# Optimization experiments

Measured on AMD Instinct MI355X. Metric: run time of the kernel, lower is better.

## Reference

```python
import jax, jax.numpy as jnp
import numpy as np

N_NODES = 50000
N_EDGES = 800000
DIM = 64
BN_EPS = 1e-5


def setup_inputs() -> dict:
    key = jax.random.key(0)
    ks = jax.random.split(key, 9)
    s = 1.0 / np.sqrt(DIM)
    feature = jax.random.normal(ks[0], (N_NODES, DIM), jnp.float32)
    edge_index = jax.random.randint(ks[1], (2, N_EDGES), 0, N_NODES)
    Wk = jax.random.normal(ks[2], (DIM, DIM), jnp.float32) * s
    Wq = jax.random.normal(ks[3], (DIM, DIM), jnp.float32) * s
    Wv = jax.random.normal(ks[4], (DIM, DIM), jnp.float32) * s
    bk = jax.random.normal(ks[5], (DIM,), jnp.float32) * 0.01
    bq = jax.random.normal(ks[6], (DIM,), jnp.float32) * 0.01
    bv = jax.random.normal(ks[7], (DIM,), jnp.float32) * 0.01
    bias = jax.random.normal(ks[8], (DIM,), jnp.float32) * 0.01
    gamma = jnp.ones((DIM,), jnp.float32)
    beta = jnp.zeros((DIM,), jnp.float32)
    return dict(feature=feature, edge_index=edge_index, Wk=Wk, bk=bk,
                Wq=Wq, bq=bq, Wv=Wv, bv=bv, bias=bias, gamma=gamma, beta=beta)


def reference(feature, edge_index, Wk, bk, Wq, bq, Wv, bv, bias, gamma, beta):
    # Node-level projections (dense GEMMs on [N, D])
    K = feature @ Wk + bk   # applied to x_i (dst)
    Q = feature @ Wq + bq   # applied to x_j (src)
    V = feature @ Wv + bv   # applied to x_j (src)
    src, dst = edge_index[0], edge_index[1]
    # Per-edge gather -> sigmoid gate -> gated message  [E, D]
    eta = jax.nn.sigmoid(K[dst] + Q[src])
    msg = eta * V[src]
    # Scatter-add into destination nodes  [N, D]
    agg = jax.ops.segment_sum(msg, dst, num_segments=feature.shape[0])
    h = agg + bias
    # BatchNorm1d over nodes (batch statistics, biased variance) + ReLU
    mean = jnp.mean(h, axis=0)
    var = jnp.var(h, axis=0)
    h = (h - mean) * jax.lax.rsqrt(var + BN_EPS) * gamma + beta
    return jax.nn.relu(h)
```

## Files before the change

kernel.cpp:

```cpp
#include <hip/hip_runtime.h>
#include <hip/hip_fp16.h>
#include <stdint.h>

#define N_NODES 50000
#define N_EDGES 800000
#define DIM 64
#define BN_EPS 1e-5f
#define CAP 64
#define ZERO_NODE N_NODES
#define POISON 0xAAAAAAAAu

#define NPTILES 391
#define FUSED_BLOCKS 1173

#define NBINS 64
#define BIN_W 784
#define BINCAP 13824

#define NTILES 3125
#define NSTATS_REP 8

typedef _Float16 f16;
typedef __attribute__((ext_vector_type(8))) _Float16 f16x8;
typedef __attribute__((ext_vector_type(4))) float f32x4;

#define LPITCH 72

__global__ __launch_bounds__(256, 4) void proj_bin_kernel(
    const float* __restrict__ feat,
    const float* __restrict__ Wk, const float* __restrict__ Wq,
    const float* __restrict__ Wv,
    const float* __restrict__ bk, const float* __restrict__ bq,
    const float* __restrict__ bv,
    __half* __restrict__ Kh, __half* __restrict__ QV,
    const int* __restrict__ ei, uint32_t* __restrict__ binCursor,
    uint32_t* __restrict__ binArr)
{
  __shared__ f16 sWt[DIM][LPITCH];
  __shared__ uint32_t hist[NBINS];
  __shared__ uint32_t gbase[NBINS];

  const int b = blockIdx.x;
  const int tid = threadIdx.x;
  const int m3 = b % 3;

  if (m3 != 0) {
    const int sid = (b / 3) * 2 + (m3 - 1);
    const int e0 = sid * 1024;
    const int e1 = (e0 + 1024 < N_EDGES) ? e0 + 1024 : N_EDGES;
    if (tid < NBINS) hist[tid] = 0;
    __syncthreads();

    int n = 0; int bn[4]; uint32_t pk[4], rk[4];
    const int base = e0 + tid * 4;
    if (base + 4 <= e1) {
      const int4 s4 = *(const int4*)(ei + base);
      const int4 d4 = *(const int4*)(ei + N_EDGES + base);
      const int ss[4] = {s4.x, s4.y, s4.z, s4.w};
      const int dd[4] = {d4.x, d4.y, d4.z, d4.w};
#pragma unroll
      for (int j = 0; j < 4; ++j) {
        const int bin = dd[j] / BIN_W;
        bn[j] = bin;
        pk[j] = (uint32_t)ss[j] | ((uint32_t)(dd[j] - bin * BIN_W) << 16);
        rk[j] = atomicAdd(&hist[bin], 1u);
      }
      n = 4;
    } else {
      for (int e = base; e < e1; ++e) {
        const int src = ei[e];
        const int dst = ei[N_EDGES + e];
        const int bin = dst / BIN_W;
        bn[n] = bin;
        pk[n] = (uint32_t)src | ((uint32_t)(dst - bin * BIN_W) << 16);
        rk[n] = atomicAdd(&hist[bin], 1u);
        ++n;
      }
    }
    __syncthreads();
    if (tid < NBINS)
      gbase[tid] = hist[tid] ? (atomicAdd(&binCursor[tid * 16], hist[tid])
                                - POISON) : 0u;
    __syncthreads();
    for (int j = 0; j < n; ++j) {
      const uint32_t pos = gbase[bn[j]] + rk[j];
      if (pos < BINCAP) binArr[(uint32_t)bn[j] * BINCAP + pos] = pk[j];
    }
    return;
  }

  const int tile0 = (b / 3) * 128;
  const int lane = tid & 63;
  const int w = tid >> 6;
  const int nl = lane & 15;
  const int kg = lane >> 4;

  f16x8 fb[2][2];
#pragma unroll
  for (int g2 = 0; g2 < 2; ++g2) {
    const int node = tile0 + w * 32 + g2 * 16 + nl;
    const bool ok = node < N_NODES;
    const float* fp = feat + (size_t)(ok ? node : 0) * DIM;
#pragma unroll
    for (int kk = 0; kk < 2; ++kk) {
      const float4 x0 = ((const float4*)(fp + kk * 32 + kg * 8))[0];
      const float4 x1 = ((const float4*)(fp + kk * 32 + kg * 8))[1];
      f16x8 r;
      r[0] = (f16)x0.x; r[1] = (f16)x0.y; r[2] = (f16)x0.z; r[3] = (f16)x0.w;
      r[4] = (f16)x1.x; r[5] = (f16)x1.y; r[6] = (f16)x1.z; r[7] = (f16)x1.w;
      if (!ok) r = (f16x8)(f16)0.f;
      fb[g2][kk] = r;
    }
  }

#pragma unroll
  for (int m = 0; m < 3; ++m) {
    const float* __restrict__ Wm = (m == 0) ? Wk : (m == 1) ? Wq : Wv;
    const float* __restrict__ bb = (m == 0) ? bk : (m == 1) ? bq : bv;

    __syncthreads();
    for (int i = tid; i < 1024; i += 256) {
      const int c = i & 63;
      const int kq = i >> 6;
      union { f16 h[4]; uint2 u; } pkw;
      pkw.h[0] = (f16)Wm[(kq * 4 + 0) * 64 + c];
      pkw.h[1] = (f16)Wm[(kq * 4 + 1) * 64 + c];
      pkw.h[2] = (f16)Wm[(kq * 4 + 2) * 64 + c];
      pkw.h[3] = (f16)Wm[(kq * 4 + 3) * 64 + c];
      *(uint2*)&sWt[c][kq * 4] = pkw.u;
    }
    __syncthreads();

    f16x8 fa[4][2];
#pragma unroll
    for (int nt = 0; nt < 4; ++nt)
#pragma unroll
      for (int kk = 0; kk < 2; ++kk)
        fa[nt][kk] = *(const f16x8*)&sWt[nt * 16 + nl][kk * 32 + kg * 8];
    f32x4 bias[4];
#pragma unroll
    for (int nt = 0; nt < 4; ++nt)
      bias[nt] = *(const f32x4*)&bb[nt * 16 + kg * 4];

#pragma unroll
    for (int g2 = 0; g2 < 2; ++g2) {
      const int node = tile0 + w * 32 + g2 * 16 + nl;
      f32x4 acc[4];
#pragma unroll
      for (int nt = 0; nt < 4; ++nt) acc[nt] = bias[nt];
#pragma unroll
      for (int kk = 0; kk < 2; ++kk)
#pragma unroll
        for (int nt = 0; nt < 4; ++nt)
          acc[nt] = __builtin_amdgcn_mfma_f32_16x16x32_f16(
              fa[nt][kk], fb[g2][kk], acc[nt], 0, 0, 0);

      if (m == 0) {
        if (node < N_NODES) {
#pragma unroll
          for (int nt = 0; nt < 4; ++nt) {
            union { __half2 h[2]; uint2 u; } pkk;
            pkk.h[0] = __floats2half2_rn(acc[nt][0], acc[nt][1]);
            pkk.h[1] = __floats2half2_rn(acc[nt][2], acc[nt][3]);
            ((uint2*)Kh)[node * 16 + nt * 4 + kg] = pkk.u;
          }
        }
      } else {
        if (node <= N_NODES) {
          const int half = (m == 1) ? 0 : 1;
#pragma unroll
          for (int nt = 0; nt < 4; ++nt) {
            union { __half2 h[2]; uint2 u; } pkk;
            pkk.h[0] = __floats2half2_rn(acc[nt][0], acc[nt][1]);
            pkk.h[1] = __floats2half2_rn(acc[nt][2], acc[nt][3]);
            if (node == N_NODES) { pkk.u.x = 0u; pkk.u.y = 0u; }
            ((uint2*)QV)[node * 32 + (nt * 4 + kg) * 2 + half] = pkk.u;
          }
        }
      }
    }
  }
}

__global__ __launch_bounds__(256) void scatter_kernel(
    const uint32_t* __restrict__ binArr, const uint32_t* __restrict__ binCursor,
    uint32_t* __restrict__ counts, uint16_t* __restrict__ bucket)
{
  __shared__ uint32_t lcnt[BIN_W];
  const int g = blockIdx.x;
  const int tid = threadIdx.x;
  for (int i = tid; i < BIN_W; i += 256) lcnt[i] = 0;
  __syncthreads();

  uint32_t cnt = binCursor[g * 16] - POISON;
  if (cnt > BINCAP) cnt = BINCAP;
  const uint32_t* arr = binArr + (uint32_t)g * BINCAP;
  const int nbase = g * BIN_W;

  for (uint32_t i = tid * 4; i < cnt; i += 1024) {
    if (i + 4 <= cnt) {
      const uint4 p4 = *(const uint4*)(arr + i);
      const uint32_t ps[4] = {p4.x, p4.y, p4.z, p4.w};
#pragma unroll
      for (int j = 0; j < 4; ++j) {
        const uint32_t dl = ps[j] >> 16;
        const uint32_t r = atomicAdd(&lcnt[dl], 1u);
        if (r < CAP)
          bucket[(size_t)(nbase + dl) * CAP + r] = (uint16_t)(ps[j] & 0xFFFFu);
      }
    } else {
      for (uint32_t e = i; e < cnt; ++e) {
        const uint32_t p = arr[e];
        const uint32_t dl = p >> 16;
        const uint32_t r = atomicAdd(&lcnt[dl], 1u);
        if (r < CAP)
          bucket[(size_t)(nbase + dl) * CAP + r] = (uint16_t)(p & 0xFFFFu);
      }
    }
  }
  __syncthreads();
  for (int i = tid; i < BIN_W; i += 256) {
    const int node = nbase + i;
    if (node < N_NODES) counts[node] = lcnt[i] + POISON;
  }
}

__device__ __forceinline__ float4 edge_acc(float4 acc, const float4 k,
                                           const uint4 qv)
{
  union { uint32_t u; __half2 h; } q0, q1, v0, v1;
  q0.u = qv.x; q1.u = qv.y; v0.u = qv.z; v1.u = qv.w;
  const float2 qa = __half22float2(q0.h);
  const float2 qb = __half22float2(q1.h);
  const float2 va = __half22float2(v0.h);
  const float2 vb = __half22float2(v1.h);
  acc.x += va.x * __builtin_amdgcn_rcpf(1.0f + __expf(-(k.x + qa.x)));
  acc.y += va.y * __builtin_amdgcn_rcpf(1.0f + __expf(-(k.y + qa.y)));
  acc.z += vb.x * __builtin_amdgcn_rcpf(1.0f + __expf(-(k.z + qb.x)));
  acc.w += vb.y * __builtin_amdgcn_rcpf(1.0f + __expf(-(k.w + qb.y)));
  return acc;
}

__global__ __launch_bounds__(256) void aggregate_kernel(
    const uint32_t* __restrict__ counts, const uint16_t* __restrict__ bucket,
    const uint2* __restrict__ Kh2, const uint4* __restrict__ QV4,
    float4* __restrict__ agg4, float* __restrict__ stats)
{
  const int tid = threadIdx.x;
  const int row = tid >> 4;
  const int t = tid & 15;
  const int n = blockIdx.x * 16 + row;

  union { uint2 u; __half2 h[2]; } kun;
  kun.u = Kh2[n * 16 + t];
  const float2 k0 = __half22float2(kun.h[0]);
  const float2 k1 = __half22float2(kun.h[1]);
  const float4 k = make_float4(k0.x, k0.y, k1.x, k1.y);

  int deg = (int)(counts[n] - POISON);
  if (deg > CAP) deg = CAP;
  const uint16_t* bp = bucket + (size_t)n * CAP;
  float4 acc = make_float4(0.f, 0.f, 0.f, 0.f);

  for (int j0 = 0; j0 < deg; j0 += 16) {
    const int navail = deg - j0;
    const int s = (t < navail) ? (int)bp[j0 + t] : ZERO_NODE;

    int sA[8]; uint4 qvA[8];
#pragma unroll
    for (int i = 0; i < 8; ++i) sA[i] = __shfl(s, i, 16);
#pragma unroll
    for (int i = 0; i < 8; ++i) qvA[i] = QV4[sA[i] * 16 + t];

    const bool haveB = navail > 8;
    int sB[8]; uint4 qvB[8];
    if (haveB) {
#pragma unroll
      for (int i = 0; i < 8; ++i) sB[i] = __shfl(s, 8 + i, 16);
#pragma unroll
      for (int i = 0; i < 8; ++i) qvB[i] = QV4[sB[i] * 16 + t];
    }

#pragma unroll
    for (int i = 0; i < 8; ++i) acc = edge_acc(acc, k, qvA[i]);
    if (haveB) {
#pragma unroll
      for (int i = 0; i < 8; ++i) acc = edge_acc(acc, k, qvB[i]);
    }
  }
  agg4[n * 16 + t] = acc;

  __shared__ float sred[2][16][DIM + 4];
  float4 pssq;
  pssq.x = acc.x * acc.x; pssq.y = acc.y * acc.y;
  pssq.z = acc.z * acc.z; pssq.w = acc.w * acc.w;
  *(float4*)&sred[0][row][t * 4] = acc;
  *(float4*)&sred[1][row][t * 4] = pssq;
  __syncthreads();
  if (tid < 128) {
    const int s = tid >> 6, c = tid & 63;
    float v = 0.0f;
#pragma unroll
    for (int r = 0; r < 16; ++r) v += sred[s][r][c];
    atomicAdd(&stats[(blockIdx.x & (NSTATS_REP - 1)) * 128 + tid], v);
  }
}

__global__ __launch_bounds__(256) void out_kernel(
    float* __restrict__ out, const float* __restrict__ stats,
    const float* __restrict__ gamma, const float* __restrict__ beta)
{
  __shared__ float sstats[128];
  const int tid = threadIdx.x;
  if (tid < 128) {
    float v = 0.0f;
#pragma unroll
    for (int r = 0; r < NSTATS_REP; ++r) v += stats[r * 128 + tid];
    sstats[tid] = v;
  }
  __syncthreads();

  const int idx = blockIdx.x * 256 + tid;
  if (idx >= N_NODES * (DIM / 4)) return;
  const int t = idx & 15;
  const float4 v = ((const float4*)out)[idx];
  const float invN = 1.0f / (float)N_NODES;
  const float vin[4] = { v.x, v.y, v.z, v.w };
  float o[4];
#pragma unroll
  for (int j = 0; j < 4; ++j) {
    const int c = t * 4 + j;
    const float mean = sstats[c] * invN;
    float var = sstats[DIM + c] * invN - mean * mean;
    var = var < 0.0f ? 0.0f : var;
    const float scale = rsqrtf(var + BN_EPS) * gamma[c];
    const float shift = beta[c] - mean * scale;
    const float x = vin[j] * scale + shift;
    o[j] = x > 0.0f ? x : 0.0f;
  }
  float4 r; r.x = o[0]; r.y = o[1]; r.z = o[2]; r.w = o[3];
  ((float4*)out)[idx] = r;
}

extern "C" void kernel_launch(void* const* d_in, const int* in_sizes, int n_in,
                              void* d_out, int out_size, void* d_ws, size_t ws_size,
                              hipStream_t stream) {
  (void)in_sizes; (void)n_in; (void)out_size; (void)ws_size;
  const float* feat  = (const float*)d_in[0];
  const int*   ei    = (const int*)d_in[1];
  const float* Wk    = (const float*)d_in[2];
  const float* bk    = (const float*)d_in[3];
  const float* Wq    = (const float*)d_in[4];
  const float* bq    = (const float*)d_in[5];
  const float* Wv    = (const float*)d_in[6];
  const float* bv    = (const float*)d_in[7];
  const float* gamma = (const float*)d_in[9];
  const float* beta  = (const float*)d_in[10];

  char* base = (char*)d_ws;
  __half*   Kh       = (__half*)base;
  __half*   QV       = (__half*)(base + 6400000);
  float*    stats    = (float*)(base + 19200256);
  uint32_t* counts   = (uint32_t*)(base + 19204352);
  uint16_t* bucket   = (uint16_t*)(base + 19404352);
  uint32_t* binCursor= (uint32_t*)(base + 25804352);
  uint32_t* binArr   = (uint32_t*)(base + 25808448);

  proj_bin_kernel<<<FUSED_BLOCKS, 256, 0, stream>>>(
      feat, Wk, Wq, Wv, bk, bq, bv, Kh, QV, ei, binCursor, binArr);

  scatter_kernel<<<NBINS, 256, 0, stream>>>(binArr, binCursor, counts, bucket);

  aggregate_kernel<<<NTILES, 256, 0, stream>>>(
      counts, bucket, (const uint2*)Kh, (const uint4*)QV, (float4*)d_out,
      stats);

  out_kernel<<<(N_NODES * (DIM / 4) + 255) / 256, 256, 0, stream>>>(
      (float*)d_out, stats, gamma, beta);
}
```

Before: 161.4 us.

## Fuse per-node bucket scatter into aggregation via smaller bins and shared-memory lists

Removes the separate scatter kernel and its global bucket/counts arrays. Bins shrink to 208 nodes, so each 16-node aggregation tile (13 tiles per bin) can scan its bin's edge list and build the per-node source lists in shared memory. This saves one kernel launch and a global write-then-read of the bucket array. In exchange, each bin's edge list is read 13 times, once by each tile, and the binning stage must handle more bins.

```diff
diff --git a/kernel.cpp b/kernel.cpp
--- a/kernel.cpp
+++ b/kernel.cpp
@@ -13,9 +13,9 @@
 #define NPTILES 391
 #define FUSED_BLOCKS 1173
 
-#define NBINS 64
-#define BIN_W 784
-#define BINCAP 13824
+#define NBINS 241
+#define BIN_W 208
+#define BINCAP 4352
 
 #define NTILES 3125
 #define NSTATS_REP 8
@@ -179,49 +179,6 @@
         }
       }
     }
-  }
-}
-
-__global__ __launch_bounds__(256) void scatter_kernel(
-    const uint32_t* __restrict__ binArr, const uint32_t* __restrict__ binCursor,
-    uint32_t* __restrict__ counts, uint16_t* __restrict__ bucket)
-{
-  __shared__ uint32_t lcnt[BIN_W];
-  const int g = blockIdx.x;
-  const int tid = threadIdx.x;
-  for (int i = tid; i < BIN_W; i += 256) lcnt[i] = 0;
-  __syncthreads();
-
-  uint32_t cnt = binCursor[g * 16] - POISON;
-  if (cnt > BINCAP) cnt = BINCAP;
-  const uint32_t* arr = binArr + (uint32_t)g * BINCAP;
-  const int nbase = g * BIN_W;
-
-  for (uint32_t i = tid * 4; i < cnt; i += 1024) {
-    if (i + 4 <= cnt) {
-      const uint4 p4 = *(const uint4*)(arr + i);
-      const uint32_t ps[4] = {p4.x, p4.y, p4.z, p4.w};
-#pragma unroll
-      for (int j = 0; j < 4; ++j) {
-        const uint32_t dl = ps[j] >> 16;
-        const uint32_t r = atomicAdd(&lcnt[dl], 1u);
-        if (r < CAP)
-          bucket[(size_t)(nbase + dl) * CAP + r] = (uint16_t)(ps[j] & 0xFFFFu);
-      }
-    } else {
-      for (uint32_t e = i; e < cnt; ++e) {
-        const uint32_t p = arr[e];
-        const uint32_t dl = p >> 16;
-        const uint32_t r = atomicAdd(&lcnt[dl], 1u);
-        if (r < CAP)
-          bucket[(size_t)(nbase + dl) * CAP + r] = (uint16_t)(p & 0xFFFFu);
-      }
-    }
-  }
-  __syncthreads();
-  for (int i = tid; i < BIN_W; i += 256) {
-    const int node = nbase + i;
-    if (node < N_NODES) counts[node] = lcnt[i] + POISON;
   }
 }
 
@@ -242,14 +199,52 @@
 }
 
 __global__ __launch_bounds__(256) void aggregate_kernel(
-    const uint32_t* __restrict__ counts, const uint16_t* __restrict__ bucket,
+    const uint32_t* __restrict__ binArr, const uint32_t* __restrict__ binCursor,
     const uint2* __restrict__ Kh2, const uint4* __restrict__ QV4,
     float4* __restrict__ agg4, float* __restrict__ stats)
 {
+  __shared__ uint16_t slist[16][CAP];
+  __shared__ uint32_t lcnt[16];
   const int tid = threadIdx.x;
+  const int tile = blockIdx.x;
+  const int g = tile / 13;
+  const uint32_t lo = (uint32_t)((tile - g * 13) * 16);
+
+  if (tid < 16) lcnt[tid] = 0;
+  __syncthreads();
+
+  uint32_t cnt = binCursor[g * 16] - POISON;
+  if (cnt > BINCAP) cnt = BINCAP;
+  const uint32_t* arr = binArr + (uint32_t)g * BINCAP;
+
+  for (uint32_t i = tid * 4; i < cnt; i += 1024) {
+    if (i + 4 <= cnt) {
+      const uint4 p4 = *(const uint4*)(arr + i);
+      const uint32_t ps[4] = {p4.x, p4.y, p4.z, p4.w};
+#pragma unroll
+      for (int j = 0; j < 4; ++j) {
+        const uint32_t idx = (ps[j] >> 16) - lo;
+        if (idx < 16u) {
+          const uint32_t r = atomicAdd(&lcnt[idx], 1u);
+          if (r < CAP) slist[idx][r] = (uint16_t)(ps[j] & 0xFFFFu);
+        }
+      }
+    } else {
+      for (uint32_t e = i; e < cnt; ++e) {
+        const uint32_t p = arr[e];
+        const uint32_t idx = (p >> 16) - lo;
+        if (idx < 16u) {
+          const uint32_t r = atomicAdd(&lcnt[idx], 1u);
+          if (r < CAP) slist[idx][r] = (uint16_t)(p & 0xFFFFu);
+        }
+      }
+    }
+  }
+  __syncthreads();
+
   const int row = tid >> 4;
   const int t = tid & 15;
-  const int n = blockIdx.x * 16 + row;
+  const int n = tile * 16 + row;
 
   union { uint2 u; __half2 h[2]; } kun;
   kun.u = Kh2[n * 16 + t];
@@ -257,14 +252,13 @@
   const float2 k1 = __half22float2(kun.h[1]);
   const float4 k = make_float4(k0.x, k0.y, k1.x, k1.y);
 
-  int deg = (int)(counts[n] - POISON);
+  int deg = (int)lcnt[row];
   if (deg > CAP) deg = CAP;
-  const uint16_t* bp = bucket + (size_t)n * CAP;
   float4 acc = make_float4(0.f, 0.f, 0.f, 0.f);
 
   for (int j0 = 0; j0 < deg; j0 += 16) {
     const int navail = deg - j0;
-    const int s = (t < navail) ? (int)bp[j0 + t] : ZERO_NODE;
+    const int s = (t < navail) ? (int)slist[row][j0 + t] : ZERO_NODE;
 
     int sA[8]; uint4 qvA[8];
 #pragma unroll
@@ -361,18 +355,14 @@
   __half*   Kh       = (__half*)base;
   __half*   QV       = (__half*)(base + 6400000);
   float*    stats    = (float*)(base + 19200256);
-  uint32_t* counts   = (uint32_t*)(base + 19204352);
-  uint16_t* bucket   = (uint16_t*)(base + 19404352);
-  uint32_t* binCursor= (uint32_t*)(base + 25804352);
-  uint32_t* binArr   = (uint32_t*)(base + 25808448);
+  uint32_t* binCursor= (uint32_t*)(base + 19204352);
+  uint32_t* binArr   = (uint32_t*)(base + 19219776);
 
   proj_bin_kernel<<<FUSED_BLOCKS, 256, 0, stream>>>(
       feat, Wk, Wq, Wv, bk, bq, bv, Kh, QV, ei, binCursor, binArr);
 
-  scatter_kernel<<<NBINS, 256, 0, stream>>>(binArr, binCursor, counts, bucket);
-
   aggregate_kernel<<<NTILES, 256, 0, stream>>>(
-      counts, bucket, (const uint2*)Kh, (const uint4*)QV, (float4*)d_out,
+      binArr, binCursor, (const uint2*)Kh, (const uint4*)QV, (float4*)d_out,
       stats);
 
   out_kernel<<<(N_NODES * (DIM / 4) + 255) / 256, 256, 0, stream>>>(
```

Result: no change. 160.3 us (-0.7%).
